# Performance work log

Measured on AMD Instinct MI355X. Metric: run time of the kernel, lower is better.

## Reference

```python
import jax, jax.numpy as jnp
from jax import lax
import numpy as np

BS, C_IN, C_OUT, STYLE_D, H, W, F = 8, 256, 256, 512, 64, 64, 3


def setup_inputs() -> dict:
    key = jax.random.key(0)
    k = jax.random.split(key, 6)
    # xavier_uniform for conv weight: gain=1, fan_in=c_in*f*f, fan_out=c_out*f*f
    fan_in, fan_out = C_IN * F * F, C_OUT * F * F
    limit_w = float(np.sqrt(6.0 / (fan_in + fan_out)))
    limit_a = float(np.sqrt(1.0 / STYLE_D))  # torch Linear default init bound
    return {
        "x": jax.random.normal(k[0], (BS, C_IN, H, W), jnp.float32),
        "s": jax.random.normal(k[1], (BS, STYLE_D), jnp.float32),
        "w": jax.random.uniform(k[2], (C_OUT, C_IN, F, F), jnp.float32, -limit_w, limit_w),
        "b": jnp.zeros((C_OUT, 1, 1), jnp.float32),
        "affine_w": jax.random.uniform(k[3], (C_IN, STYLE_D), jnp.float32, -limit_a, limit_a),
        "affine_b": jax.random.uniform(k[4], (C_IN,), jnp.float32, -limit_a, limit_a),
    }


def reference(x, s, w, b, affine_w, affine_b):
    bs = x.shape[0]
    # style -> per-channel modulation scales: [bs, c_in]
    style = s @ affine_w.T + affine_b
    # modulate: [bs, c_out, c_in, f, f]
    wmod = w[None, :, :, :, :] * (style[:, None, :, None, None] + 1.0)
    # demodulate
    d = jnp.sqrt(jnp.sum(jnp.square(wmod), axis=(2, 3, 4), keepdims=True) + 1e-8)
    wmod = wmod / d
    # grouped conv with groups=bs (per-sample weights)
    xr = x.reshape(1, bs * x.shape[1], x.shape[2], x.shape[3])
    cw = wmod.reshape(bs * wmod.shape[1], wmod.shape[2], wmod.shape[3], wmod.shape[4])
    out = lax.conv_general_dilated(
        xr, cw, window_strides=(1, 1), padding=((1, 1), (1, 1)),
        dimension_numbers=("NCHW", "OIHW", "NCHW"), feature_group_count=bs)
    out = out.reshape(bs, wmod.shape[1], out.shape[2], out.shape[3])
    return out + b  # b broadcasts as [c_out,1,1]
```

## Files before the change

### kernel.cpp

```cpp
#include <hip/hip_runtime.h>
#include <hip/hip_bf16.h>
#include <stdint.h>

#define BS   8
#define CIN  256
#define COUT 256
#define SD   512
#define HH   64
#define WW   64
#define HP   66

typedef __attribute__((ext_vector_type(8))) short short8;
typedef __attribute__((ext_vector_type(4))) float f32x4;

__device__ __forceinline__ unsigned short f2bf(float f) {
    __hip_bfloat16 h = __float2bfloat16(f);
    return *reinterpret_cast<unsigned short*>(&h);
}

typedef __attribute__((address_space(3))) unsigned int lds_u32_t;
typedef const __attribute__((address_space(1))) unsigned int glb_u32_t;

__device__ __forceinline__ void async16(const void* g, void* l) {
    __builtin_amdgcn_global_load_lds((glb_u32_t*)g, (lds_u32_t*)l, 16, 0, 0);
}

__global__ void k_style(const float* __restrict__ s, const float* __restrict__ aw,
                        const float* __restrict__ ab, float* __restrict__ m) {
    int b = blockIdx.x >> 3, chunk = blockIdx.x & 7;
    int tid = threadIdx.x;
    __shared__ float sv[SD];
    for (int d = tid; d < SD; d += 256) sv[d] = s[b * SD + d];
    __syncthreads();
    int il = tid >> 3, p = tid & 7;
    int i = chunk * 32 + il;
    const float4* awr = (const float4*)(aw + (size_t)i * SD + p * 64);
    float acc = 0.f;
#pragma unroll
    for (int d4 = 0; d4 < 16; ++d4) {
        float4 w4 = awr[d4];
        int d0 = p * 64 + d4 * 4;
        acc += w4.x * sv[d0] + w4.y * sv[d0 + 1] + w4.z * sv[d0 + 2] + w4.w * sv[d0 + 3];
    }
    acc += __shfl_xor(acc, 1);
    acc += __shfl_xor(acc, 2);
    acc += __shfl_xor(acc, 4);
    if (p == 0) m[b * CIN + i] = acc + ab[i] + 1.0f;
}

__global__ void k_prep(const float* __restrict__ w, const float* __restrict__ m,
                       const float* __restrict__ x,
                       unsigned short* __restrict__ wb, float* __restrict__ dinv,
                       unsigned short* __restrict__ xp) {
    __shared__ float red[4][8];
    int tid = threadIdx.x;

    if (blockIdx.x < COUT) {
        int o = blockIdx.x, i = tid;
        const float* wp = w + ((size_t)o * CIN + i) * 9;
        float v[9];
        float q = 0.f;
#pragma unroll
        for (int t = 0; t < 9; ++t) { v[t] = wp[t]; q += v[t] * v[t]; }
#pragma unroll
        for (int t = 0; t < 9; ++t)
            wb[((size_t)t * COUT + o) * CIN + i] = f2bf(v[t]);

        float r[8];
#pragma unroll
        for (int b = 0; b < 8; ++b) {
            float mv = m[b * CIN + i];
            r[b] = q * mv * mv;
        }
#pragma unroll
        for (int b = 0; b < 8; ++b) {
            r[b] += __shfl_xor(r[b], 1);
            r[b] += __shfl_xor(r[b], 2);
            r[b] += __shfl_xor(r[b], 4);
            r[b] += __shfl_xor(r[b], 8);
            r[b] += __shfl_xor(r[b], 16);
            r[b] += __shfl_xor(r[b], 32);
        }
        int lane = i & 63, wid = i >> 6;
        if (lane == 0) {
#pragma unroll
            for (int b = 0; b < 8; ++b) red[wid][b] = r[b];
        }
        __syncthreads();
        if (i < 8) {
            float acc = red[0][i] + red[1][i] + red[2][i] + red[3][i];
            dinv[i * COUT + o] = rsqrtf(acc + 1e-8f);
        }
        return;
    }

    int bi = blockIdx.x - COUT;
    int b = bi / HP, yp = bi % HP;
    unsigned short* row = xp + ((size_t)(b * HP + yp)) * HP * CIN;

    if (yp == 0 || yp == HP - 1) {
        uint4 z = {0u, 0u, 0u, 0u};
        uint4* r = (uint4*)row;
        for (int j = tid; j < HP * CIN / 8; j += 256) r[j] = z;
        return;
    }
    int y = yp - 1;

    if (tid < 64) {
        uint4 z = {0u, 0u, 0u, 0u};
        if (tid < 32) ((uint4*)row)[tid] = z;
        else ((uint4*)(row + (size_t)(HP - 1) * CIN))[tid - 32] = z;
    }

#pragma unroll
    for (int it = 0; it < 2; ++it) {
        int u = it * 256 + tid;
        int x0 = (u & 15) * 4;
        int i0 = (u >> 4) * 8;
        float vv[8][4];
        float mv[8];
#pragma unroll
        for (int k = 0; k < 8; ++k) {
            *(float4*)vv[k] = *(const float4*)&x[(((size_t)b * CIN + i0 + k) * HH + y) * WW + x0];
            mv[k] = m[b * CIN + i0 + k];
        }
#pragma unroll
        for (int j = 0; j < 4; ++j) {
            short8 p;
#pragma unroll
            for (int k = 0; k < 8; ++k)
                p[k] = (short)f2bf(vv[k][j] * mv[k]);
            *(short8*)&row[(size_t)(x0 + j + 1) * CIN + i0] = p;
        }
    }
}

__global__ void __launch_bounds__(512, 2)
k_conv(const unsigned short* __restrict__ xp,
       const unsigned short* __restrict__ wb,
       const float* __restrict__ dinv,
       const float* __restrict__ bias,
       float* __restrict__ out) {
    __shared__ unsigned short Ar[3168 * 8];
    __shared__ unsigned short Bs[4608 * 8];

    int bx = blockIdx.x;
    int mt = bx & 127;
    int n0 = (bx >> 7) << 6;
    int m0 = mt << 8;
    int b  = m0 >> 12;
    int y0 = (m0 >> 6) & 63;

    int tid = threadIdx.x;
    int lane = tid & 63, w = tid >> 6;
    int wm = w >> 1, wn = w & 1;
    int quad = lane >> 4, mrow = lane & 15;

    f32x4 acc[4][2] = {};

    const unsigned short* xb = xp + (size_t)b * HP * HP * CIN;

    auto stageA = [&](int kc) {
        int ch0 = kc * 64;
#pragma unroll
        for (int k = 0; k < 6; ++k) {
            int sA = k * 512 + tid;
            int rowA = sA / 528;
            int rem = sA - rowA * 528;
            int colA = rem >> 3, c4 = rem & 7;
            async16(xb + ((size_t)(y0 + rowA) * HP + colA) * CIN + ch0 + ((c4 ^ (colA & 7)) << 3),
                    &Ar[sA * 8]);
        }
        if (tid < 96) {
            int sA = 3072 + tid;
            int rowA = sA / 528;
            int rem = sA - rowA * 528;
            int colA = rem >> 3, c4 = rem & 7;
            async16(xb + ((size_t)(y0 + rowA) * HP + colA) * CIN + ch0 + ((c4 ^ (colA & 7)) << 3),
                    &Ar[sA * 8]);
        }
    };

    auto stageBall = [&](int kc) {
#pragma unroll
        for (int k = 0; k < 9; ++k) {
            int rowB = tid >> 3, c4 = tid & 7;
            async16(wb + ((size_t)k * COUT + n0 + rowB) * CIN + kc * 64 + ((c4 ^ (rowB & 7)) << 3),
                    &Bs[(k * 512 + tid) * 8]);
        }
    };

#pragma unroll 1
    for (int kc = 0; kc < 4; ++kc) {
        if (kc) __syncthreads();
        stageA(kc);
        stageBall(kc);
        __syncthreads();

#pragma unroll
        for (int t = 0; t < 9; ++t) {
            int dy = t / 3, dx = t - dy * 3;
            int arow = wm + dy;

            short8 af[2][4], bf[2][2];
#pragma unroll
            for (int h = 0; h < 2; ++h)
#pragma unroll
                for (int i = 0; i < 4; ++i) {
                    int col = mrow + i * 16 + dx;
                    int chunk = arow * 528 + col * 8 + ((h * 4 + quad) ^ (col & 7));
                    af[h][i] = *(const short8*)&Ar[chunk * 8];
                }
#pragma unroll
            for (int h = 0; h < 2; ++h)
#pragma unroll
                for (int j = 0; j < 2; ++j) {
                    int rowB = wn * 32 + mrow + j * 16;
                    int chunk = t * 512 + rowB * 8 + ((h * 4 + quad) ^ (rowB & 7));
                    bf[h][j] = *(const short8*)&Bs[chunk * 8];
                }
#pragma unroll
            for (int h = 0; h < 2; ++h)
#pragma unroll
                for (int i = 0; i < 4; ++i)
#pragma unroll
                    for (int j = 0; j < 2; ++j)
                        acc[i][j] = __builtin_amdgcn_mfma_f32_16x16x32_bf16(
                            af[h][i], bf[h][j], acc[i][j], 0, 0, 0);
        }
    }

    int y = y0 + wm;
#pragma unroll
    for (int j = 0; j < 2; ++j) {
        int o = n0 + wn * 32 + mrow + j * 16;
        float dv = dinv[b * COUT + o];
        float bv = bias[o];
#pragma unroll
        for (int i = 0; i < 4; ++i) {
            int xx = i * 16 + quad * 4;
            f32x4 v = acc[i][j] * dv + bv;
            *(f32x4*)(out + (((size_t)(b * COUT + o) * HH + y) * WW + xx)) = v;
        }
    }
}

extern "C" void kernel_launch(void* const* d_in, const int* in_sizes, int n_in,
                              void* d_out, int out_size, void* d_ws, size_t ws_size,
                              hipStream_t stream) {
    const float* x    = (const float*)d_in[0];
    const float* s    = (const float*)d_in[1];
    const float* w    = (const float*)d_in[2];
    const float* bias = (const float*)d_in[3];
    const float* aw   = (const float*)d_in[4];
    const float* ab   = (const float*)d_in[5];
    float* out = (float*)d_out;

    char* ws = (char*)d_ws;
    float* m            = (float*)(ws + 0);
    float* dinv         = (float*)(ws + 8192);
    unsigned short* wb  = (unsigned short*)(ws + 16384);
    unsigned short* xpb = (unsigned short*)(ws + 1196032);

    k_style<<<64, 256, 0, stream>>>(s, aw, ab, m);
    k_prep<<<COUT + BS * HP, 256, 0, stream>>>(w, m, x, wb, dinv, xpb);
    k_conv<<<512, 512, 0, stream>>>(xpb, wb, dinv, bias, out);
}
```

Before: 144.7 us.

## Enlarge conv tile to 8 rows per block and double-buffer fragment loads

Each block now covers 8 output rows × 64 cols × 64 out-channels, with each wave owning a full row and all 64 channels (4x4 MFMA accumulators), halving the grid to 256 blocks. The A halo tile grows to 10 padded rows, so there is less halo reload and B weights are reused across more rows. The 9-tap inner loop is manually software-pipelined with two register sets so LDS reads for tap t+1 overlap the MFMAs of tap t. The cost is higher register and LDS use (about 84KB LDS), which may cut occupancy below the 2 blocks per CU that the launch bounds ask for, and 256 blocks roughly matches the CU count, leaving less latency hiding.

```diff
diff --git a/kernel.cpp b/kernel.cpp
--- a/kernel.cpp
+++ b/kernel.cpp
@@ -141,29 +141,27 @@
        const float* __restrict__ dinv,
        const float* __restrict__ bias,
        float* __restrict__ out) {
-    __shared__ unsigned short Ar[3168 * 8];
+    __shared__ unsigned short Ar[5280 * 8];
     __shared__ unsigned short Bs[4608 * 8];
 
     int bx = blockIdx.x;
-    int mt = bx & 127;
-    int n0 = (bx >> 7) << 6;
-    int m0 = mt << 8;
-    int b  = m0 >> 12;
-    int y0 = (m0 >> 6) & 63;
+    int mt = bx & 63;
+    int n0 = (bx >> 6) << 6;
+    int b  = mt >> 3;
+    int y0 = (mt & 7) << 3;
 
     int tid = threadIdx.x;
     int lane = tid & 63, w = tid >> 6;
-    int wm = w >> 1, wn = w & 1;
     int quad = lane >> 4, mrow = lane & 15;
 
-    f32x4 acc[4][2] = {};
+    f32x4 acc[4][4] = {};
 
     const unsigned short* xb = xp + (size_t)b * HP * HP * CIN;
 
     auto stageA = [&](int kc) {
         int ch0 = kc * 64;
 #pragma unroll
-        for (int k = 0; k < 6; ++k) {
+        for (int k = 0; k < 10; ++k) {
             int sA = k * 512 + tid;
             int rowA = sA / 528;
             int rem = sA - rowA * 528;
@@ -171,8 +169,8 @@
             async16(xb + ((size_t)(y0 + rowA) * HP + colA) * CIN + ch0 + ((c4 ^ (colA & 7)) << 3),
                     &Ar[sA * 8]);
         }
-        if (tid < 96) {
-            int sA = 3072 + tid;
+        if (tid < 160) {
+            int sA = 5120 + tid;
             int rowA = sA / 528;
             int rem = sA - rowA * 528;
             int colA = rem >> 3, c4 = rem & 7;
@@ -189,6 +187,44 @@
                     &Bs[(k * 512 + tid) * 8]);
         }
     };
+
+#define LDA_(T, H, I) \
+    (*(const short8*)&Ar[(size_t)((w + (T) / 3) * 528 + (mrow + (I) * 16 + (T) % 3) * 8 + \
+        (((H) * 4 + quad) ^ ((mrow + (I) * 16 + (T) % 3) & 7))) * 8])
+#define LDB_(T, H, J) \
+    (*(const short8*)&Bs[(size_t)((T) * 512 + (mrow + (J) * 16) * 8 + \
+        (((H) * 4 + quad) ^ ((mrow + (J) * 16) & 7))) * 8])
+
+#define LOADSET(S, T) do { \
+    S##A0 = LDA_(T, 0, 0); S##A1 = LDA_(T, 0, 1); S##A2 = LDA_(T, 0, 2); S##A3 = LDA_(T, 0, 3); \
+    S##A4 = LDA_(T, 1, 0); S##A5 = LDA_(T, 1, 1); S##A6 = LDA_(T, 1, 2); S##A7 = LDA_(T, 1, 3); \
+    S##B0 = LDB_(T, 0, 0); S##B1 = LDB_(T, 0, 1); S##B2 = LDB_(T, 0, 2); S##B3 = LDB_(T, 0, 3); \
+    S##B4 = LDB_(T, 1, 0); S##B5 = LDB_(T, 1, 1); S##B6 = LDB_(T, 1, 2); S##B7 = LDB_(T, 1, 3); } while (0)
+
+#define MFMA1(a, bb, c) __builtin_amdgcn_mfma_f32_16x16x32_bf16(a, bb, c, 0, 0, 0)
+
+#define MFMASET(S) do { \
+    acc[0][0] = MFMA1(S##A0, S##B0, acc[0][0]); acc[0][1] = MFMA1(S##A0, S##B1, acc[0][1]); \
+    acc[0][2] = MFMA1(S##A0, S##B2, acc[0][2]); acc[0][3] = MFMA1(S##A0, S##B3, acc[0][3]); \
+    acc[1][0] = MFMA1(S##A1, S##B0, acc[1][0]); acc[1][1] = MFMA1(S##A1, S##B1, acc[1][1]); \
+    acc[1][2] = MFMA1(S##A1, S##B2, acc[1][2]); acc[1][3] = MFMA1(S##A1, S##B3, acc[1][3]); \
+    acc[2][0] = MFMA1(S##A2, S##B0, acc[2][0]); acc[2][1] = MFMA1(S##A2, S##B1, acc[2][1]); \
+    acc[2][2] = MFMA1(S##A2, S##B2, acc[2][2]); acc[2][3] = MFMA1(S##A2, S##B3, acc[2][3]); \
+    acc[3][0] = MFMA1(S##A3, S##B0, acc[3][0]); acc[3][1] = MFMA1(S##A3, S##B1, acc[3][1]); \
+    acc[3][2] = MFMA1(S##A3, S##B2, acc[3][2]); acc[3][3] = MFMA1(S##A3, S##B3, acc[3][3]); \
+    acc[0][0] = MFMA1(S##A4, S##B4, acc[0][0]); acc[0][1] = MFMA1(S##A4, S##B5, acc[0][1]); \
+    acc[0][2] = MFMA1(S##A4, S##B6, acc[0][2]); acc[0][3] = MFMA1(S##A4, S##B7, acc[0][3]); \
+    acc[1][0] = MFMA1(S##A5, S##B4, acc[1][0]); acc[1][1] = MFMA1(S##A5, S##B5, acc[1][1]); \
+    acc[1][2] = MFMA1(S##A5, S##B6, acc[1][2]); acc[1][3] = MFMA1(S##A5, S##B7, acc[1][3]); \
+    acc[2][0] = MFMA1(S##A6, S##B4, acc[2][0]); acc[2][1] = MFMA1(S##A6, S##B5, acc[2][1]); \
+    acc[2][2] = MFMA1(S##A6, S##B6, acc[2][2]); acc[2][3] = MFMA1(S##A6, S##B7, acc[2][3]); \
+    acc[3][0] = MFMA1(S##A7, S##B4, acc[3][0]); acc[3][1] = MFMA1(S##A7, S##B5, acc[3][1]); \
+    acc[3][2] = MFMA1(S##A7, S##B6, acc[3][2]); acc[3][3] = MFMA1(S##A7, S##B7, acc[3][3]); } while (0)
+
+    short8 PA0, PA1, PA2, PA3, PA4, PA5, PA6, PA7;
+    short8 PB0, PB1, PB2, PB3, PB4, PB5, PB6, PB7;
+    short8 QA0, QA1, QA2, QA3, QA4, QA5, QA6, QA7;
+    short8 QB0, QB1, QB2, QB3, QB4, QB5, QB6, QB7;
 
 #pragma unroll 1
     for (int kc = 0; kc < 4; ++kc) {
@@ -197,43 +233,28 @@
         stageBall(kc);
         __syncthreads();
 
-#pragma unroll
-        for (int t = 0; t < 9; ++t) {
-            int dy = t / 3, dx = t - dy * 3;
-            int arow = wm + dy;
-
-            short8 af[2][4], bf[2][2];
-#pragma unroll
-            for (int h = 0; h < 2; ++h)
-#pragma unroll
-                for (int i = 0; i < 4; ++i) {
-                    int col = mrow + i * 16 + dx;
-                    int chunk = arow * 528 + col * 8 + ((h * 4 + quad) ^ (col & 7));
-                    af[h][i] = *(const short8*)&Ar[chunk * 8];
-                }
-#pragma unroll
-            for (int h = 0; h < 2; ++h)
-#pragma unroll
-                for (int j = 0; j < 2; ++j) {
-                    int rowB = wn * 32 + mrow + j * 16;
-                    int chunk = t * 512 + rowB * 8 + ((h * 4 + quad) ^ (rowB & 7));
-                    bf[h][j] = *(const short8*)&Bs[chunk * 8];
-                }
-#pragma unroll
-            for (int h = 0; h < 2; ++h)
-#pragma unroll
-                for (int i = 0; i < 4; ++i)
-#pragma unroll
-                    for (int j = 0; j < 2; ++j)
-                        acc[i][j] = __builtin_amdgcn_mfma_f32_16x16x32_bf16(
-                            af[h][i], bf[h][j], acc[i][j], 0, 0, 0);
-        }
-    }
-
-    int y = y0 + wm;
-#pragma unroll
-    for (int j = 0; j < 2; ++j) {
-        int o = n0 + wn * 32 + mrow + j * 16;
+        LOADSET(P, 0);
+        LOADSET(Q, 1); MFMASET(P);
+        LOADSET(P, 2); MFMASET(Q);
+        LOADSET(Q, 3); MFMASET(P);
+        LOADSET(P, 4); MFMASET(Q);
+        LOADSET(Q, 5); MFMASET(P);
+        LOADSET(P, 6); MFMASET(Q);
+        LOADSET(Q, 7); MFMASET(P);
+        LOADSET(P, 8); MFMASET(Q);
+        MFMASET(P);
+    }
+
+#undef MFMASET
+#undef MFMA1
+#undef LOADSET
+#undef LDB_
+#undef LDA_
+
+    int y = y0 + w;
+#pragma unroll
+    for (int j = 0; j < 4; ++j) {
+        int o = n0 + mrow + j * 16;
         float dv = dinv[b * COUT + o];
         float bv = bias[o];
 #pragma unroll
@@ -264,5 +285,5 @@
 
     k_style<<<64, 256, 0, stream>>>(s, aw, ab, m);
     k_prep<<<COUT + BS * HP, 256, 0, stream>>>(w, m, x, wb, dinv, xpb);
-    k_conv<<<512, 512, 0, stream>>>(xpb, wb, dinv, bias, out);
-}
+    k_conv<<<256, 512, 0, stream>>>(xpb, wb, dinv, bias, out);
+}
```

Result: no change. 143.1 us (-1.1%).
